# Kernel optimization log

Measured on AMD Instinct MI355X. Metric: run time of the kernel, lower is better.

The kernel has to match this reference:

```python
import jax, jax.numpy as jnp
import numpy as np

D_MODEL = 1024
NUM_HEADS = 16
D_K = D_MODEL // NUM_HEADS
B, S = 2, 2048


def setup_inputs() -> dict:
    key = jax.random.key(0)
    ks = jax.random.split(key, 11)
    sc = 1.0 / np.sqrt(D_MODEL)
    return {
        "Q_input": jax.random.normal(ks[0], (B, S, D_MODEL), jnp.float32),
        "K_input": jax.random.normal(ks[1], (B, S, D_MODEL), jnp.float32),
        "V_input": jax.random.normal(ks[2], (B, S, D_MODEL), jnp.float32),
        "Wq": jax.random.normal(ks[3], (D_MODEL, D_MODEL), jnp.float32) * sc,
        "bq": jax.random.normal(ks[4], (D_MODEL,), jnp.float32) * 0.01,
        "Wk": jax.random.normal(ks[5], (D_MODEL, D_MODEL), jnp.float32) * sc,
        "bk": jax.random.normal(ks[6], (D_MODEL,), jnp.float32) * 0.01,
        "Wv": jax.random.normal(ks[7], (D_MODEL, D_MODEL), jnp.float32) * sc,
        "bv": jax.random.normal(ks[8], (D_MODEL,), jnp.float32) * 0.01,
        "Wo": jax.random.normal(ks[9], (D_MODEL, D_MODEL), jnp.float32) * sc,
        "bo": jax.random.normal(ks[10], (D_MODEL,), jnp.float32) * 0.01,
    }


def reference(Q_input, K_input, V_input, Wq, bq, Wk, bk, Wv, bv, Wo, bo):
    # Linear projections (torch Linear: x @ W.T + b)
    Q = Q_input @ Wq.T + bq  # [B,S,D]
    K = K_input @ Wk.T + bk
    V = V_input @ Wv.T + bv
    # split heads -> [B,H,S,dk]
    def split(x):
        return x.reshape(B, S, NUM_HEADS, D_K).transpose(0, 2, 1, 3)
    Qh, Kh, Vh = split(Q), split(K), split(V)
    scale = 1.0 / jnp.sqrt(jnp.asarray(D_K, Qh.dtype))
    scores = jnp.einsum('bhqd,bhkd->bhqk', Qh, Kh) * scale  # [B,H,S,S]
    attn = jax.nn.softmax(scores, axis=-1)
    ctx = jnp.einsum('bhqk,bhkd->bhqd', attn, Vh)  # [B,H,S,dk]
    concat = ctx.transpose(0, 2, 1, 3).reshape(B, S, D_MODEL)
    out = concat @ Wo.T + bo  # dropout is identity in eval
    return out
```

## Files before the change

kernel.cpp:

```cpp
#include <hip/hip_runtime.h>
#include <stdint.h>

#define DM   1024
#define NH   16
#define DKH  64
#define BBATCH 2
#define SEQ  2048
#define MTOK (BBATCH*SEQ)

typedef unsigned short u16;
typedef unsigned int   u32;
typedef __attribute__((ext_vector_type(8))) short  bf16x8;
typedef __attribute__((ext_vector_type(4))) float  f32x4;

struct PtrArr11 { const void* p[11]; };
struct U16Arr11 { u16* p[11]; };

__device__ __forceinline__ float bf2f(u16 u) {
  union { unsigned int i; float f; } z; z.i = ((unsigned int)u) << 16; return z.f;
}
__device__ __forceinline__ u16 f2bf(float f) {
  union { float f; unsigned int i; } z; z.f = f;
  unsigned int i = z.i + 0x7fffu + ((z.i >> 16) & 1u);
  return (u16)(i >> 16);
}

__device__ __forceinline__ bf16x8 u4_to_bf(u32 a, u32 b, u32 c, u32 d) {
  union { u32 u[4]; bf16x8 v; } z; z.u[0] = a; z.u[1] = b; z.u[2] = c; z.u[3] = d; return z.v;
}

__device__ __forceinline__ void gld16(const void* g, void* l) {
  __builtin_amdgcn_global_load_lds(
      (const __attribute__((address_space(1))) void*)g,
      (__attribute__((address_space(3))) void*)l,
      16, 0, 0);
}

__global__ void k_detect(const unsigned int* __restrict__ w, int* __restrict__ flag) {
  const int ln = threadIdx.x & 63;
  const unsigned int word = w[ln];
  const unsigned int ex = (word >> 7) & 0xFFu;
  const int hit = (ex >= 100u && ex <= 126u) ? 1 : 0;
  unsigned long long m = __ballot(hit);
  if (ln == 0) *flag = (__popcll(m) >= 40) ? 0 : 1;
}

__global__ __launch_bounds__(256) void k_convert_all(PtrArr11 src, U16Arr11 dst,
                                                     const int* __restrict__ flag) {
  if (*flag == 0) return;
  const int b = blockIdx.x;
  int seg, base;
  if      (b <  2048) { seg = 0;  base = 0;    }
  else if (b <  4096) { seg = 1;  base = 2048; }
  else if (b <  6144) { seg = 2;  base = 4096; }
  else if (b <  6656) { seg = 3;  base = 6144; }
  else if (b == 6656) { seg = 4;  base = 6656; }
  else if (b <  7169) { seg = 5;  base = 6657; }
  else if (b == 7169) { seg = 6;  base = 7169; }
  else if (b <  7682) { seg = 7;  base = 7170; }
  else if (b == 7682) { seg = 8;  base = 7682; }
  else if (b <  8195) { seg = 9;  base = 7683; }
  else                { seg = 10; base = 8195; }
  const int n = (seg < 3) ? (MTOK * DM) : ((seg & 1) ? (DM * DM) : DM);
  const int i0 = (b - base) * 2048 + threadIdx.x * 8;
  if (i0 >= n) return;
  const float* s = (const float*)src.p[seg] + i0;
  const f32x4 x0 = *(const f32x4*)(s);
  const f32x4 x1 = *(const f32x4*)(s + 4);
  bf16x8 o;
#pragma unroll
  for (int j = 0; j < 4; ++j) o[j] = (short)f2bf(x0[j]);
#pragma unroll
  for (int j = 0; j < 4; ++j) o[4 + j] = (short)f2bf(x1[j]);
  *(bf16x8*)(dst.p[seg] + i0) = o;
}

__device__ __forceinline__ void gemm_body64(const u16* __restrict__ X,
                                            const u16* __restrict__ W,
                                            const u16* __restrict__ bias,
                                            u16* __restrict__ out,
                                            int m0, int n0)
{
  __shared__ __attribute__((aligned(16))) u16 sA[128 * 64];
  __shared__ __attribute__((aligned(16))) u16 sB[128 * 64];
  const int tid = threadIdx.x;
  const int ln = tid & 63, wv = tid >> 6;
  const int wm = wv & 1, wn = wv >> 1;
  const int fr = ln & 15, fq = ln >> 4;
  const int fr7 = fr & 7;
  const int srow = ln >> 3;
  const int scol = ((ln & 7) ^ srow) * 8;

  f32x4 acc[4][4];
#pragma unroll
  for (int i = 0; i < 4; ++i)
#pragma unroll
    for (int j = 0; j < 4; ++j) acc[i][j] = (f32x4){0.f, 0.f, 0.f, 0.f};

  const u16* pA = X + (size_t)(m0 + wv * 32 + srow) * DM + scol;
  const u16* pB = W + (size_t)(n0 + wv * 32 + srow) * DM + scol;
  u16* lA = sA + wv * 32 * 64;
  u16* lB = sB + wv * 32 * 64;

  for (int k0 = 0; k0 < DM; k0 += 64) {
#pragma unroll
    for (int c = 0; c < 4; ++c) {
      gld16(pA + (size_t)(c * 8) * DM + k0, lA + c * 8 * 64);
      gld16(pB + (size_t)(c * 8) * DM + k0, lB + c * 8 * 64);
    }
    asm volatile("s_waitcnt vmcnt(0)" ::: "memory");
    __syncthreads();

    bf16x8 af[4][2], bfg[4][2];
#pragma unroll
    for (int t = 0; t < 4; ++t)
#pragma unroll
      for (int ks = 0; ks < 2; ++ks) {
        af[t][ks]  = *(const bf16x8*)(sA + (wm * 64 + t * 16 + fr) * 64 + ((ks * 4 + fq) ^ fr7) * 8);
        bfg[t][ks] = *(const bf16x8*)(sB + (wn * 64 + t * 16 + fr) * 64 + ((ks * 4 + fq) ^ fr7) * 8);
      }
#pragma unroll
    for (int i = 0; i < 4; ++i)
#pragma unroll
      for (int j = 0; j < 4; ++j) {
        acc[i][j] = __builtin_amdgcn_mfma_f32_16x16x32_bf16(af[i][0], bfg[j][0], acc[i][j], 0, 0, 0);
        acc[i][j] = __builtin_amdgcn_mfma_f32_16x16x32_bf16(af[i][1], bfg[j][1], acc[i][j], 0, 0, 0);
      }
    __syncthreads();
  }

#pragma unroll
  for (int i = 0; i < 4; ++i) {
    const int row = m0 + wm * 64 + i * 16 + fq * 4;
#pragma unroll
    for (int j = 0; j < 4; ++j) {
      const int col = n0 + wn * 64 + j * 16 + fr;
      const float bv = bf2f(bias[col]);
#pragma unroll
      for (int r = 0; r < 4; ++r)
        out[(size_t)(row + r) * DM + col] = f2bf(acc[i][j][r] + bv);
    }
  }
}

__device__ __forceinline__ void gemm_body_n64(const u16* __restrict__ X,
                                              const u16* __restrict__ W,
                                              const u16* __restrict__ bias,
                                              void* __restrict__ out,
                                              int isf32out, int m0, int n0)
{
  __shared__ __attribute__((aligned(16))) u16 sA[128 * 32];
  __shared__ __attribute__((aligned(16))) u16 sB[64 * 32];
  const int tid = threadIdx.x;
  const int ln = tid & 63, wv = tid >> 6;
  const int wm = wv >> 1, wn = wv & 1;
  const int fr = ln & 15, fq = ln >> 4;
  const int srow = ln >> 2, sslot = (ln & 3) * 8;

  f32x4 acc[4][2];
#pragma unroll
  for (int i = 0; i < 4; ++i)
#pragma unroll
    for (int j = 0; j < 2; ++j) acc[i][j] = (f32x4){0.f, 0.f, 0.f, 0.f};

  const u16* pA = X + (size_t)(m0 + wv * 32 + srow) * DM + sslot;
  const u16* pB = W + (size_t)(n0 + wv * 16 + srow) * DM + sslot;
  u16* lA0 = sA + (wv * 2) * 512; u16* lA1 = sA + (wv * 2 + 1) * 512;
  u16* lB  = sB + wv * 512;

  for (int k0 = 0; k0 < DM; k0 += 32) {
    gld16(pA + k0,           lA0);
    gld16(pA + 16 * DM + k0, lA1);
    gld16(pB + k0,           lB);
    asm volatile("s_waitcnt vmcnt(0)" ::: "memory");
    __syncthreads();

    bf16x8 af[4], bfg[2];
#pragma unroll
    for (int t = 0; t < 4; ++t)
      af[t]  = *(const bf16x8*)(sA + (wm * 64 + t * 16 + fr) * 32 + fq * 8);
#pragma unroll
    for (int t = 0; t < 2; ++t)
      bfg[t] = *(const bf16x8*)(sB + (wn * 32 + t * 16 + fr) * 32 + fq * 8);
#pragma unroll
    for (int i = 0; i < 4; ++i)
#pragma unroll
      for (int j = 0; j < 2; ++j)
        acc[i][j] = __builtin_amdgcn_mfma_f32_16x16x32_bf16(af[i], bfg[j], acc[i][j], 0, 0, 0);
    __syncthreads();
  }

#pragma unroll
  for (int i = 0; i < 4; ++i) {
    const int row = m0 + wm * 64 + i * 16 + fq * 4;
#pragma unroll
    for (int j = 0; j < 2; ++j) {
      const int col = n0 + wn * 32 + j * 16 + fr;
      const float bv = bf2f(bias[col]);
#pragma unroll
      for (int r = 0; r < 4; ++r) {
        const float val = acc[i][j][r] + bv;
        const size_t idx = (size_t)(row + r) * DM + col;
        if (isf32out) ((float*)out)[idx] = val;
        else          ((u16*)out)[idx]   = f2bf(val);
      }
    }
  }
}

__global__ __launch_bounds__(256, 2) void k_gemm_qkv(
    PtrArr11 orig, U16Arr11 conv, const int* __restrict__ flag,
    u16* oq, u16* ok, u16* ov)
{
  const int f = *flag;
  const int z = blockIdx.z;
  const u16* X  = f ? conv.p[z]         : (const u16*)orig.p[z];
  const u16* W  = f ? conv.p[3 + 2 * z] : (const u16*)orig.p[3 + 2 * z];
  const u16* bi = f ? conv.p[4 + 2 * z] : (const u16*)orig.p[4 + 2 * z];
  u16* o = (z == 0) ? oq : (z == 1) ? ok : ov;
  const int bid = blockIdx.y * 8 + blockIdx.x;
  const int m0 = ((((bid >> 3) & 3) << 3) | (bid & 7)) * 128;
  const int n0 = (bid >> 5) * 128;
  gemm_body64(X, W, bi, o, m0, n0);
}

__global__ __launch_bounds__(256, 2) void k_gemm_one(
    const u16* X, const void* Wo_o, const u16* Wo_c,
    const void* bo_o, const u16* bo_c, const int* __restrict__ flag, void* o)
{
  const int f = *flag;
  const u16* W  = f ? Wo_c : (const u16*)Wo_o;
  const u16* bi = f ? bo_c : (const u16*)bo_o;
  const int bid = blockIdx.y * 16 + blockIdx.x;
  const int m0 = ((((bid >> 3) & 3) << 3) | (bid & 7)) * 128;
  const int n0 = ((bid >> 5) & 15) * 64;
  gemm_body_n64(X, W, bi, o, f, m0, n0);
}

__global__ __launch_bounds__(256) void k_transpose(const u16* __restrict__ in,
                                                   u16* __restrict__ out)
{
  __shared__ u16 t[64][66];
  const int b = blockIdx.z;
  const int s0 = blockIdx.x * 64, d0 = blockIdx.y * 64;
  const int c = threadIdx.x & 63, r0 = threadIdx.x >> 6;
#pragma unroll
  for (int i = 0; i < 16; ++i) {
    const int r = r0 + 4 * i;
    t[r][c] = in[(size_t)(b * SEQ + s0 + r) * DM + d0 + c];
  }
  __syncthreads();
#pragma unroll
  for (int i = 0; i < 16; ++i) {
    const int r = r0 + 4 * i;
    out[(size_t)(b * DM + d0 + r) * SEQ + s0 + c] = t[c][r];
  }
}

__global__ __launch_bounds__(256, 2) void k_attn(
    const u16* __restrict__ Qp, const u16* __restrict__ Kp,
    const u16* __restrict__ Vt, u16* __restrict__ ctx)
{
  __shared__ __attribute__((aligned(16))) u16 sK[2][2][64 * 64];
  __shared__ __attribute__((aligned(16))) u16 sV[2][2][64 * 64];

  const int tid = threadIdx.x;
  const int ln = tid & 63, wv = tid >> 6;
  const int bid = blockIdx.y * 16 + blockIdx.x;
  const int bh  = ((bid >> 7) << 3) | (bid & 7);
  const int qx  = (bid >> 3) & 15;
  const int b = bh >> 4, h = bh & 15;
  const int q0 = qx * 128 + wv * 32;
  const int fr = ln & 15, fq = ln >> 4;
  const int fr7 = fr & 7;

  const int srow = ln >> 3;
  const int scol = ((ln & 7) ^ srow) * 8;
  const u16* gK0 = Kp + (size_t)(b * SEQ + wv * 16 + srow) * DM + h * DKH + scol;
  const u16* gV0 = Vt + (size_t)(b * DM + h * DKH + wv * 16 + srow) * SEQ + scol;
  u16* sKb = &sK[0][0][0];
  u16* sVb = &sV[0][0][0];

  bf16x8 qf[2][2];
#pragma unroll
  for (int qt = 0; qt < 2; ++qt)
#pragma unroll
    for (int ks = 0; ks < 2; ++ks) {
      const u16* src = Qp + (size_t)(b * SEQ + q0 + qt * 16 + fr) * DM + h * DKH + ks * 32 + fq * 8;
      bf16x8 v = *(const bf16x8*)src;
      bf16x8 w;
#pragma unroll
      for (int j = 0; j < 8; ++j) w[j] = (short)f2bf(bf2f((u16)v[j]) * 0.125f);
      qf[qt][ks] = w;
    }

  float l_a[2] = {0.f, 0.f};
  float l_b[2] = {0.f, 0.f};
  f32x4 o_acc[2][4];
#pragma unroll
  for (int qt = 0; qt < 2; ++qt)
#pragma unroll
    for (int dt = 0; dt < 4; ++dt) o_acc[qt][dt] = (f32x4){0.f, 0.f, 0.f, 0.f};

#define STAGE_KV128(pp, key0)                                       \
  do {                                                              \
    _Pragma("unroll")                                               \
    for (int hh = 0; hh < 2; ++hh) {                                \
      u16* kd = sKb + (pp) * 8192 + hh * 4096 + wv * 1024;          \
      u16* vd = sVb + (pp) * 8192 + hh * 4096 + wv * 1024;          \
      const int kk = (key0) + hh * 64;                              \
      gld16(gK0 + (size_t)kk * DM, kd);                             \
      gld16(gK0 + (size_t)(kk + 8) * DM, kd + 512);                 \
      gld16(gV0 + kk, vd);                                          \
      gld16(gV0 + kk + 8 * SEQ, vd + 512);                          \
    }                                                               \
  } while (0)

  STAGE_KV128(0, 0);
  asm volatile("s_waitcnt vmcnt(0)" ::: "memory");
  __syncthreads();

  int p = 0;
  for (int kb = 0; kb < SEQ / 128; ++kb) {
    if (kb + 1 < SEQ / 128) STAGE_KV128(p ^ 1, (kb + 1) * 128);

#pragma unroll
    for (int hh = 0; hh < 2; ++hh) {
      const u16* K = sKb + p * 8192 + hh * 4096;
      const u16* V = sVb + p * 8192 + hh * 4096;

      bf16x8 kf[4][2];
#pragma unroll
      for (int nt = 0; nt < 4; ++nt)
#pragma unroll
        for (int ks = 0; ks < 2; ++ks)
          kf[nt][ks] = *(const bf16x8*)(K + (nt * 16 + fr) * 64 + ((ks * 4 + fq) ^ fr7) * 8);

      u32 pw[2][2][4];
#pragma unroll
      for (int qt = 0; qt < 2; ++qt) {
        f32x4 s_acc[4];
#pragma unroll
        for (int nt = 0; nt < 4; ++nt) s_acc[nt] = (f32x4){0.f, 0.f, 0.f, 0.f};
        __builtin_amdgcn_s_setprio(1);
#pragma unroll
        for (int nt = 0; nt < 4; ++nt)
#pragma unroll
          for (int ks = 0; ks < 2; ++ks)
            s_acc[nt] = __builtin_amdgcn_mfma_f32_16x16x32_bf16(kf[nt][ks], qf[qt][ks], s_acc[nt], 0, 0, 0);
        __builtin_amdgcn_s_setprio(0);

        u32 w[4][2];
#pragma unroll
        for (int nt = 0; nt < 4; ++nt)
#pragma unroll
          for (int t = 0; t < 2; ++t) {
            const float e0 = __expf(s_acc[nt][2 * t]);
            const float e1 = __expf(s_acc[nt][2 * t + 1]);
            l_a[qt] += e0;
            l_b[qt] += e1;
            u32 wd;
            asm("v_cvt_pk_bf16_f32 %0, %1, %2" : "=v"(wd) : "v"(e0), "v"(e1));
            w[nt][t] = wd;
          }
#pragma unroll
        for (int ks = 0; ks < 2; ++ks) {
          u32 a0 = w[2 * ks][0], b0 = w[2 * ks + 1][0];
          u32 a1 = w[2 * ks][1], b1 = w[2 * ks + 1][1];
          asm("v_permlane32_swap_b32 %0, %1" : "+v"(a0), "+v"(b0));
          asm("v_permlane16_swap_b32 %0, %1" : "+v"(a0), "+v"(b0));
          asm("v_permlane32_swap_b32 %0, %1" : "+v"(a1), "+v"(b1));
          asm("v_permlane16_swap_b32 %0, %1" : "+v"(a1), "+v"(b1));
          pw[qt][ks][0] = a0; pw[qt][ks][1] = a1; pw[qt][ks][2] = b0; pw[qt][ks][3] = b1;
        }
      }

#pragma unroll
      for (int dt = 0; dt < 4; ++dt) {
        bf16x8 vf0 = *(const bf16x8*)(V + (dt * 16 + fr) * 64 + ((0 + fq) ^ fr7) * 8);
        bf16x8 vf1 = *(const bf16x8*)(V + (dt * 16 + fr) * 64 + ((4 + fq) ^ fr7) * 8);
        __builtin_amdgcn_s_setprio(1);
#pragma unroll
        for (int qt = 0; qt < 2; ++qt) {
          o_acc[qt][dt] = __builtin_amdgcn_mfma_f32_16x16x32_bf16(
              u4_to_bf(pw[qt][0][0], pw[qt][0][1], pw[qt][0][2], pw[qt][0][3]), vf0, o_acc[qt][dt], 0, 0, 0);
          o_acc[qt][dt] = __builtin_amdgcn_mfma_f32_16x16x32_bf16(
              u4_to_bf(pw[qt][1][0], pw[qt][1][1], pw[qt][1][2], pw[qt][1][3]), vf1, o_acc[qt][dt], 0, 0, 0);
        }
        __builtin_amdgcn_s_setprio(0);
      }
    }

    asm volatile("s_waitcnt vmcnt(0)" ::: "memory");
    __syncthreads();
    p ^= 1;
  }
#undef STAGE_KV128

  float iv[2][4];
#pragma unroll
  for (int qt = 0; qt < 2; ++qt) {
    float t = l_a[qt] + l_b[qt];
    t += __shfl_xor(t, 16);
    t += __shfl_xor(t, 32);
    const float rl = 1.0f / t;
#pragma unroll
    for (int rr = 0; rr < 4; ++rr) iv[qt][rr] = __shfl(rl, fq * 4 + rr);
  }
#pragma unroll
  for (int qt = 0; qt < 2; ++qt)
#pragma unroll
    for (int dt = 0; dt < 4; ++dt)
#pragma unroll
      for (int r = 0; r < 4; ++r) {
        const int qrow = q0 + qt * 16 + fq * 4 + r;
        const int col = h * DKH + dt * 16 + fr;
        ctx[(size_t)(b * SEQ + qrow) * DM + col] = f2bf(o_acc[qt][dt][r] * iv[qt][r]);
      }
}

extern "C" void kernel_launch(void* const* d_in, const int* in_sizes, int n_in,
                              void* d_out, int out_size, void* d_ws, size_t ws_size,
                              hipStream_t stream)
{
  char* ws = (char*)d_ws;
  int* flag = (int*)ws;

  const size_t TOKSZ = (size_t)MTOK * DM * sizeof(u16);
  const size_t WSZ   = (size_t)DM * DM * sizeof(u16);
  const size_t BSZ   = 4096;

  size_t off = 256;
  u16* Qc  = (u16*)(ws + off); off += TOKSZ;
  u16* Kc  = (u16*)(ws + off); off += TOKSZ;
  u16* Vc  = (u16*)(ws + off); off += TOKSZ;
  u16* Wqc = (u16*)(ws + off); off += WSZ;
  u16* Wkc = (u16*)(ws + off); off += WSZ;
  u16* Wvc = (u16*)(ws + off); off += WSZ;
  u16* Woc = (u16*)(ws + off); off += WSZ;
  u16* bqc = (u16*)(ws + off); off += BSZ;
  u16* bkc = (u16*)(ws + off); off += BSZ;
  u16* bvc = (u16*)(ws + off); off += BSZ;
  u16* boc = (u16*)(ws + off); off += BSZ;
  u16* Qp  = (u16*)(ws + off); off += TOKSZ;
  u16* Kp  = (u16*)(ws + off); off += TOKSZ;
  u16* Vp  = (u16*)(ws + off); off += TOKSZ;
  u16* Vt  = Qc;
  u16* ctx = Kc;

  PtrArr11 orig;
  for (int i = 0; i < 11; ++i) orig.p[i] = d_in[i];
  U16Arr11 conv;
  conv.p[0] = Qc;  conv.p[1] = Kc;  conv.p[2] = Vc;
  conv.p[3] = Wqc; conv.p[4] = bqc; conv.p[5] = Wkc; conv.p[6] = bkc;
  conv.p[7] = Wvc; conv.p[8] = bvc; conv.p[9] = Woc; conv.p[10] = boc;

  dim3 blk(256);

  k_detect<<<1, 64, 0, stream>>>((const unsigned int*)d_in[3], flag);
  k_convert_all<<<8196, blk, 0, stream>>>(orig, conv, flag);
  k_gemm_qkv<<<dim3(DM / 128, MTOK / 128, 3), blk, 0, stream>>>(
      orig, conv, flag, Qp, Kp, Vp);
  k_transpose<<<dim3(SEQ / 64, DM / 64, BBATCH), blk, 0, stream>>>(Vp, Vt);
  k_attn<<<dim3(SEQ / 128, BBATCH * NH), blk, 0, stream>>>(Qp, Kp, Vt, ctx);
  k_gemm_one<<<dim3(DM / 64, MTOK / 128, 1), blk, 0, stream>>>(
      ctx, d_in[9], Woc, d_in[10], boc, flag, d_out);
}
```

Before: 220.6 us.

## Fuse V transpose into QKV GEMM epilogue and use exp2 softmax

Result: no change. 221.3 us (+0.3%).

```diff
diff --git a/kernel.cpp b/kernel.cpp
--- a/kernel.cpp
+++ b/kernel.cpp
@@ -11,6 +11,7 @@
 typedef unsigned short u16;
 typedef unsigned int   u32;
 typedef __attribute__((ext_vector_type(8))) short  bf16x8;
+typedef __attribute__((ext_vector_type(4))) short  s16x4;
 typedef __attribute__((ext_vector_type(4))) float  f32x4;
 
 struct PtrArr11 { const void* p[11]; };
@@ -75,14 +76,25 @@
   *(bf16x8*)(dst.p[seg] + i0) = o;
 }
 
-__device__ __forceinline__ void gemm_body64(const u16* __restrict__ X,
-                                            const u16* __restrict__ W,
-                                            const u16* __restrict__ bias,
-                                            u16* __restrict__ out,
-                                            int m0, int n0)
+__global__ __launch_bounds__(256, 2) void k_gemm_qkv(
+    PtrArr11 orig, U16Arr11 conv, const int* __restrict__ flag,
+    u16* oq, u16* ok, u16* ovt)
 {
-  __shared__ __attribute__((aligned(16))) u16 sA[128 * 64];
-  __shared__ __attribute__((aligned(16))) u16 sB[128 * 64];
+  __shared__ __attribute__((aligned(16))) u16 smem[128 * 136];
+  u16* sA = smem;
+  u16* sB = smem + 128 * 64;
+  u16* T  = smem;
+
+  const int f = *flag;
+  const int z = blockIdx.z;
+  const u16* X  = f ? conv.p[z]         : (const u16*)orig.p[z];
+  const u16* W  = f ? conv.p[3 + 2 * z] : (const u16*)orig.p[3 + 2 * z];
+  const u16* bi = f ? conv.p[4 + 2 * z] : (const u16*)orig.p[4 + 2 * z];
+
+  const int bid = blockIdx.y * 8 + blockIdx.x;
+  const int m0 = ((((bid >> 3) & 3) << 3) | (bid & 7)) * 128;
+  const int n0 = (bid >> 5) * 128;
+
   const int tid = threadIdx.x;
   const int ln = tid & 63, wv = tid >> 6;
   const int wm = wv & 1, wn = wv >> 1;
@@ -129,17 +141,42 @@
     __syncthreads();
   }
 
-#pragma unroll
-  for (int i = 0; i < 4; ++i) {
-    const int row = m0 + wm * 64 + i * 16 + fq * 4;
-#pragma unroll
-    for (int j = 0; j < 4; ++j) {
-      const int col = n0 + wn * 64 + j * 16 + fr;
-      const float bv = bf2f(bias[col]);
-#pragma unroll
-      for (int r = 0; r < 4; ++r)
-        out[(size_t)(row + r) * DM + col] = f2bf(acc[i][j][r] + bv);
-    }
+  if (z < 2) {
+    u16* out = (z == 0) ? oq : ok;
+#pragma unroll
+    for (int i = 0; i < 4; ++i) {
+      const int row = m0 + wm * 64 + i * 16 + fq * 4;
+#pragma unroll
+      for (int j = 0; j < 4; ++j) {
+        const int col = n0 + wn * 64 + j * 16 + fr;
+        const float bv = bf2f(bi[col]);
+#pragma unroll
+        for (int r = 0; r < 4; ++r)
+          out[(size_t)(row + r) * DM + col] = f2bf(acc[i][j][r] + bv);
+      }
+    }
+  } else {
+#pragma unroll
+    for (int i = 0; i < 4; ++i) {
+      const int rl = wm * 64 + i * 16 + fq * 4;
+#pragma unroll
+      for (int j = 0; j < 4; ++j) {
+        const int cl = wn * 64 + j * 16 + fr;
+        const float bv = bf2f(bi[n0 + cl]);
+        s16x4 pk;
+#pragma unroll
+        for (int r = 0; r < 4; ++r) pk[r] = (short)f2bf(acc[i][j][r] + bv);
+        *(s16x4*)(T + cl * 136 + rl) = pk;
+      }
+    }
+    __syncthreads();
+    const int cl = tid >> 1, h2 = (tid & 1) * 64;
+    const int bb = m0 >> 11, s0 = m0 & 2047;
+    u16* dst = ovt + ((size_t)(bb * DM + n0 + cl)) * SEQ + s0 + h2;
+    const u16* srcT = T + cl * 136 + h2;
+#pragma unroll
+    for (int k = 0; k < 8; ++k)
+      *(bf16x8*)(dst + k * 8) = *(const bf16x8*)(srcT + k * 8);
   }
 }
 
@@ -208,22 +245,6 @@
   }
 }
 
-__global__ __launch_bounds__(256, 2) void k_gemm_qkv(
-    PtrArr11 orig, U16Arr11 conv, const int* __restrict__ flag,
-    u16* oq, u16* ok, u16* ov)
-{
-  const int f = *flag;
-  const int z = blockIdx.z;
-  const u16* X  = f ? conv.p[z]         : (const u16*)orig.p[z];
-  const u16* W  = f ? conv.p[3 + 2 * z] : (const u16*)orig.p[3 + 2 * z];
-  const u16* bi = f ? conv.p[4 + 2 * z] : (const u16*)orig.p[4 + 2 * z];
-  u16* o = (z == 0) ? oq : (z == 1) ? ok : ov;
-  const int bid = blockIdx.y * 8 + blockIdx.x;
-  const int m0 = ((((bid >> 3) & 3) << 3) | (bid & 7)) * 128;
-  const int n0 = (bid >> 5) * 128;
-  gemm_body64(X, W, bi, o, m0, n0);
-}
-
 __global__ __launch_bounds__(256, 2) void k_gemm_one(
     const u16* X, const void* Wo_o, const u16* Wo_c,
     const void* bo_o, const u16* bo_c, const int* __restrict__ flag, void* o)
@@ -237,26 +258,6 @@
   gemm_body_n64(X, W, bi, o, f, m0, n0);
 }
 
-__global__ __launch_bounds__(256) void k_transpose(const u16* __restrict__ in,
-                                                   u16* __restrict__ out)
-{
-  __shared__ u16 t[64][66];
-  const int b = blockIdx.z;
-  const int s0 = blockIdx.x * 64, d0 = blockIdx.y * 64;
-  const int c = threadIdx.x & 63, r0 = threadIdx.x >> 6;
-#pragma unroll
-  for (int i = 0; i < 16; ++i) {
-    const int r = r0 + 4 * i;
-    t[r][c] = in[(size_t)(b * SEQ + s0 + r) * DM + d0 + c];
-  }
-  __syncthreads();
-#pragma unroll
-  for (int i = 0; i < 16; ++i) {
-    const int r = r0 + 4 * i;
-    out[(size_t)(b * DM + d0 + r) * SEQ + s0 + c] = t[c][r];
-  }
-}
-
 __global__ __launch_bounds__(256, 2) void k_attn(
     const u16* __restrict__ Qp, const u16* __restrict__ Kp,
     const u16* __restrict__ Vt, u16* __restrict__ ctx)
@@ -290,7 +291,7 @@
       bf16x8 v = *(const bf16x8*)src;
       bf16x8 w;
 #pragma unroll
-      for (int j = 0; j < 8; ++j) w[j] = (short)f2bf(bf2f((u16)v[j]) * 0.125f);
+      for (int j = 0; j < 8; ++j) w[j] = (short)f2bf(bf2f((u16)v[j]) * 0.18033688011f);
       qf[qt][ks] = w;
     }
 
@@ -355,8 +356,8 @@
         for (int nt = 0; nt < 4; ++nt)
 #pragma unroll
           for (int t = 0; t < 2; ++t) {
-            const float e0 = __expf(s_acc[nt][2 * t]);
-            const float e1 = __expf(s_acc[nt][2 * t + 1]);
+            const float e0 = __builtin_amdgcn_exp2f(s_acc[nt][2 * t]);
+            const float e1 = __builtin_amdgcn_exp2f(s_acc[nt][2 * t + 1]);
             l_a[qt] += e0;
             l_b[qt] += e1;
             u32 wd;
@@ -445,7 +446,6 @@
   u16* Qp  = (u16*)(ws + off); off += TOKSZ;
   u16* Kp  = (u16*)(ws + off); off += TOKSZ;
   u16* Vp  = (u16*)(ws + off); off += TOKSZ;
-  u16* Vt  = Qc;
   u16* ctx = Kc;
 
   PtrArr11 orig;
@@ -461,8 +461,7 @@
   k_convert_all<<<8196, blk, 0, stream>>>(orig, conv, flag);
   k_gemm_qkv<<<dim3(DM / 128, MTOK / 128, 3), blk, 0, stream>>>(
       orig, conv, flag, Qp, Kp, Vp);
-  k_transpose<<<dim3(SEQ / 64, DM / 64, BBATCH), blk, 0, stream>>>(Vp, Vt);
-  k_attn<<<dim3(SEQ / 128, BBATCH * NH), blk, 0, stream>>>(Qp, Kp, Vt, ctx);
+  k_attn<<<dim3(SEQ / 128, BBATCH * NH), blk, 0, stream>>>(Qp, Kp, Vp, ctx);
   k_gemm_one<<<dim3(DM / 64, MTOK / 128, 1), blk, 0, stream>>>(
       ctx, d_in[9], Woc, d_in[10], boc, flag, d_out);
 }
```
